# Optimization experiments

Measured on AMD Instinct MI355X. Metric: run time of the kernel, lower is better.

## Reference

```python
import math
import jax, jax.numpy as jnp
import numpy as np

B, S, D, H = 2, 2048, 1024, 16
DK = D // H


def setup_inputs() -> dict:
    key = jax.random.key(0)
    ks = jax.random.split(key, 12)
    scale = 1.0 / math.sqrt(D)
    inp = {
        "q": jax.random.normal(ks[0], (B, S, D), jnp.float32),
        "k": jax.random.normal(ks[1], (B, S, D), jnp.float32),
        "v": jax.random.normal(ks[2], (B, S, D), jnp.float32),
        # causal mask, broadcast over batch and heads (mask==0 -> -inf)
        "mask": jnp.tril(jnp.ones((S, S), jnp.int32))[None, None, :, :],
        "Wq": jax.random.normal(ks[3], (D, D), jnp.float32) * scale,
        "bq": jnp.zeros((D,), jnp.float32),
        "Wk": jax.random.normal(ks[4], (D, D), jnp.float32) * scale,
        "bk": jnp.zeros((D,), jnp.float32),
        "Wv": jax.random.normal(ks[5], (D, D), jnp.float32) * scale,
        "bv": jnp.zeros((D,), jnp.float32),
        "Wo": jax.random.normal(ks[6], (D, D), jnp.float32) * scale,
        "bo": jnp.zeros((D,), jnp.float32),
    }
    return inp


def reference(q, k, v, mask, Wq, bq, Wk, bk, Wv, bv, Wo, bo):
    def proj(x, W, b):
        # [B,S,D] -> [B,H,S,DK]
        return (x @ W + b).reshape(B, -1, H, DK).transpose(0, 2, 1, 3)

    Q = proj(q, Wq, bq)
    K = proj(k, Wk, bk)
    V = proj(v, Wv, bv)
    scores = jnp.einsum("bhqd,bhkd->bhqk", Q, K) / math.sqrt(DK)  # [B,H,S,S]
    scores = jnp.where(mask == 0, -jnp.inf, scores)
    attn = jax.nn.softmax(scores, axis=-1)  # dropout p=0.0 -> identity
    ctx = jnp.einsum("bhqk,bhkd->bhqd", attn, V)
    ctx = ctx.transpose(0, 2, 1, 3).reshape(B, -1, D)  # [B,S,D]
    return ctx @ Wo + bo
```

## Files before the change

### kernel.cpp

```cpp
#include <hip/hip_runtime.h>
#include <stdint.h>

#define BB 2
#define SS 2048
#define DD 1024
#define HH 16
#define DK 64

#define QSCALE 0.1803368801111204f
#define NEGS -1.0e30f

typedef short s16x8 __attribute__((ext_vector_type(8)));
typedef float f32x4 __attribute__((ext_vector_type(4)));
typedef unsigned short u16x4 __attribute__((ext_vector_type(4)));
typedef unsigned int u32x4 __attribute__((ext_vector_type(4)));

static __device__ __forceinline__ unsigned short f2bf(float f) {
  unsigned int u = __builtin_bit_cast(unsigned int, f);
  u = (u + 0x7fffu + ((u >> 16) & 1u)) >> 16;
  return (unsigned short)u;
}

static __device__ __forceinline__ unsigned int cvtpk(float lo, float hi) {
  unsigned int r;
  asm("v_cvt_pk_bf16_f32 %0, %1, %2" : "=v"(r) : "v"(lo), "v"(hi));
  return r;
}

static __device__ __forceinline__ f32x4 mfma16(s16x8 a, s16x8 b, f32x4 c) {
  return __builtin_amdgcn_mfma_f32_16x16x32_bf16(a, b, c, 0, 0, 0);
}

static __device__ __forceinline__ void gload_lds16(const void* g, void* l) {
  __builtin_amdgcn_global_load_lds(
      (const __attribute__((address_space(1))) unsigned int*)g,
      (__attribute__((address_space(3))) unsigned int*)l, 16, 0, 0);
}

__global__ __launch_bounds__(256) void cvt3_kernel(const float* __restrict__ q,
                                                   const float* __restrict__ k,
                                                   const float* __restrict__ v,
                                                   unsigned short* __restrict__ qb,
                                                   unsigned short* __restrict__ kb,
                                                   unsigned short* __restrict__ vb) {
  int sel = blockIdx.y;
  const float* in = (sel == 0) ? q : ((sel == 1) ? k : v);
  unsigned short* out = (sel == 0) ? qb : ((sel == 1) ? kb : vb);
  int i = blockIdx.x * 256 + threadIdx.x;
  f32x4 vv = ((const f32x4*)in)[i];
  u16x4 o;
  o.x = f2bf(vv.x); o.y = f2bf(vv.y); o.z = f2bf(vv.z); o.w = f2bf(vv.w);
  ((u16x4*)out)[i] = o;
}

__global__ __launch_bounds__(256) void transpose_w4_kernel(const float* __restrict__ Wq,
                                                           const float* __restrict__ Wk,
                                                           const float* __restrict__ Wv,
                                                           const float* __restrict__ Wo,
                                                           unsigned short* __restrict__ WTbase) {
  __shared__ float t[32][33];
  int z = blockIdx.z;
  const float* W = (z == 0) ? Wq : ((z == 1) ? Wk : ((z == 2) ? Wv : Wo));
  float scale = (z == 0) ? QSCALE : 1.0f;
  unsigned short* WT = WTbase + (size_t)z * DD * DD;
  int n0 = blockIdx.x * 32, k0 = blockIdx.y * 32;
  int tx = threadIdx.x, ty = threadIdx.y;
  for (int i = 0; i < 4; ++i)
    t[ty + 8 * i][tx] = W[(size_t)(k0 + ty + 8 * i) * DD + n0 + tx];
  __syncthreads();
  for (int i = 0; i < 4; ++i)
    WT[(size_t)(n0 + ty + 8 * i) * DD + k0 + tx] = f2bf(t[tx][ty + 8 * i] * scale);
}

__global__ __launch_bounds__(256) void transpose_v_kernel(const unsigned short* __restrict__ V,
                                                          unsigned short* __restrict__ VT) {
  __shared__ unsigned short t[32][33];
  int s0 = blockIdx.x * 32, d0 = blockIdx.y * 32, bh = blockIdx.z;
  int tx = threadIdx.x, ty = threadIdx.y;
  const unsigned short* Vb = V + (size_t)bh * SS * DK;
  unsigned short* Tb = VT + (size_t)bh * DK * SS;
  for (int i = 0; i < 4; ++i)
    t[ty + 8 * i][tx] = Vb[(size_t)(s0 + ty + 8 * i) * DK + d0 + tx];
  __syncthreads();
  for (int i = 0; i < 4; ++i)
    Tb[(size_t)(d0 + ty + 8 * i) * SS + s0 + tx] = t[tx][ty + 8 * i];
}

__global__ __launch_bounds__(256) void gemm_qkv_kernel(
    const unsigned short* __restrict__ qb, const unsigned short* __restrict__ kb,
    const unsigned short* __restrict__ vb, const unsigned short* __restrict__ WTbase,
    const float* __restrict__ bq, const float* __restrict__ bk,
    const float* __restrict__ bv, unsigned short* __restrict__ Qh,
    unsigned short* __restrict__ Kh, unsigned short* __restrict__ Vh) {
  const int K = DD;
  __shared__ __align__(16) unsigned short Alds[128 * 32];
  __shared__ __align__(16) unsigned short Blds[128 * 32];
  int tid = threadIdx.x;
  int lane = tid & 63, wave = tid >> 6;
  int g = lane >> 4, r16 = lane & 15;
  int seg = blockIdx.y >> 5;
  int m0 = (blockIdx.y & 31) * 128, n0 = blockIdx.x * 128;
  int wm = (wave >> 1) * 64, wn = (wave & 1) * 64;

  const unsigned short* A = (seg == 0) ? qb : ((seg == 1) ? kb : vb);
  const unsigned short* BT = WTbase + (size_t)seg * DD * DD;
  const float* bias = (seg == 0) ? bq : ((seg == 1) ? bk : bv);
  unsigned short* outh = (seg == 0) ? Qh : ((seg == 1) ? Kh : Vh);
  float bsc = (seg == 0) ? QSCALE : 1.0f;

  f32x4 acc[4][4] = {};

  int c0 = tid, c1 = tid + 256;
  int arow0 = c0 >> 2, arow1 = c1 >> 2;
  int as0 = (c0 & 3) ^ ((arow0 >> 1) & 3);
  int as1 = (c1 & 3) ^ ((arow1 >> 1) & 3);

  for (int k0 = 0; k0 < K; k0 += 32) {
    __syncthreads();
    gload_lds16((const char*)(A + (size_t)(m0 + arow0) * K + k0) + as0 * 16,
                (char*)Alds + wave * 1024);
    gload_lds16((const char*)(A + (size_t)(m0 + arow1) * K + k0) + as1 * 16,
                (char*)Alds + wave * 1024 + 4096);
    gload_lds16((const char*)(BT + (size_t)(n0 + arow0) * K + k0) + as0 * 16,
                (char*)Blds + wave * 1024);
    gload_lds16((const char*)(BT + (size_t)(n0 + arow1) * K + k0) + as1 * 16,
                (char*)Blds + wave * 1024 + 4096);
    __syncthreads();

    s16x8 af[4], bfr[4];
#pragma unroll
    for (int mt = 0; mt < 4; ++mt) {
      int row = wm + mt * 16 + r16;
      int ch = g ^ ((row >> 1) & 3);
      af[mt] = *(const s16x8*)((const char*)Alds + row * 64 + ch * 16);
    }
#pragma unroll
    for (int nt = 0; nt < 4; ++nt) {
      int row = wn + nt * 16 + r16;
      int ch = g ^ ((row >> 1) & 3);
      bfr[nt] = *(const s16x8*)((const char*)Blds + row * 64 + ch * 16);
    }
#pragma unroll
    for (int mt = 0; mt < 4; ++mt)
#pragma unroll
      for (int nt = 0; nt < 4; ++nt)
        acc[mt][nt] = mfma16(af[mt], bfr[nt], acc[mt][nt]);
  }

#pragma unroll
  for (int nt = 0; nt < 4; ++nt) {
    int col = n0 + wn + nt * 16 + r16;
    int h = col >> 6, dk = col & (DK - 1);
    float bvv = bias[col] * bsc;
#pragma unroll
    for (int mt = 0; mt < 4; ++mt) {
#pragma unroll
      for (int rr = 0; rr < 4; ++rr) {
        int rowg = m0 + wm + mt * 16 + g * 4 + rr;
        int bb = rowg >> 11, s = rowg & (SS - 1);
        float val = acc[mt][nt][rr] + bvv;
        outh[(((size_t)bb * HH + h) * SS + s) * DK + dk] = f2bf(val);
      }
    }
  }
}

__global__ __launch_bounds__(256) void gemm_out_kernel(const unsigned short* __restrict__ A,
                                                       const unsigned short* __restrict__ BT,
                                                       const float* __restrict__ bias,
                                                       float* __restrict__ out) {
  const int K = DD;
  __shared__ __align__(16) unsigned short Alds[128 * 32];
  __shared__ __align__(16) unsigned short Blds[64 * 32];
  int tid = threadIdx.x;
  int lane = tid & 63, wave = tid >> 6;
  int g = lane >> 4, r16 = lane & 15;
  int m0 = blockIdx.y * 128, n0 = blockIdx.x * 64;
  int wm = (wave >> 1) * 64, wn = (wave & 1) * 32;

  f32x4 acc[4][2] = {};

  int c0 = tid, c1 = tid + 256;
  int arow0 = c0 >> 2, arow1 = c1 >> 2;
  int as0 = (c0 & 3) ^ ((arow0 >> 1) & 3);
  int as1 = (c1 & 3) ^ ((arow1 >> 1) & 3);

  for (int k0 = 0; k0 < K; k0 += 32) {
    __syncthreads();
    gload_lds16((const char*)(A + (size_t)(m0 + arow0) * K + k0) + as0 * 16,
                (char*)Alds + wave * 1024);
    gload_lds16((const char*)(A + (size_t)(m0 + arow1) * K + k0) + as1 * 16,
                (char*)Alds + wave * 1024 + 4096);
    gload_lds16((const char*)(BT + (size_t)(n0 + arow0) * K + k0) + as0 * 16,
                (char*)Blds + wave * 1024);
    __syncthreads();

    s16x8 af[4], bfr[2];
#pragma unroll
    for (int mt = 0; mt < 4; ++mt) {
      int row = wm + mt * 16 + r16;
      int ch = g ^ ((row >> 1) & 3);
      af[mt] = *(const s16x8*)((const char*)Alds + row * 64 + ch * 16);
    }
#pragma unroll
    for (int nt = 0; nt < 2; ++nt) {
      int row = wn + nt * 16 + r16;
      int ch = g ^ ((row >> 1) & 3);
      bfr[nt] = *(const s16x8*)((const char*)Blds + row * 64 + ch * 16);
    }
#pragma unroll
    for (int mt = 0; mt < 4; ++mt)
#pragma unroll
      for (int nt = 0; nt < 2; ++nt)
        acc[mt][nt] = mfma16(af[mt], bfr[nt], acc[mt][nt]);
  }

#pragma unroll
  for (int nt = 0; nt < 2; ++nt) {
    int col = n0 + wn + nt * 16 + r16;
    float bvv = bias[col];
#pragma unroll
    for (int mt = 0; mt < 4; ++mt) {
#pragma unroll
      for (int rr = 0; rr < 4; ++rr) {
        int rowg = m0 + wm + mt * 16 + g * 4 + rr;
        out[(size_t)rowg * DD + col] = acc[mt][nt][rr] + bvv;
      }
    }
  }
}

__global__ __launch_bounds__(256) void attn_kernel(const unsigned short* __restrict__ Qh,
                                                   const unsigned short* __restrict__ Kh,
                                                   const unsigned short* __restrict__ VhT,
                                                   unsigned short* __restrict__ ctx) {
  __shared__ __align__(16) unsigned short Klds[3][64 * 64];
  __shared__ __align__(16) unsigned short Vlds[3][64 * 64];

  int tid = threadIdx.x;
  int lane = tid & 63, wave = tid >> 6;
  int g = lane >> 4, r16 = lane & 15;
  int bid = blockIdx.x;
  int bh = ((bid >> 7) << 3) | (bid & 7);
  int pid = (bid >> 3) & 15;

  const int NTQ = SS / 64;
  int q0A = pid * 64, q0B = (NTQ - 1 - pid) * 64;
  int tilesA = pid + 1;
  int NT = NTQ + 1;

  const unsigned short* Qb = Qh + (size_t)bh * SS * DK;
  const char* Kb = (const char*)(Kh + (size_t)bh * SS * DK);
  const char* Vb = (const char*)(VhT + (size_t)bh * DK * SS);

  int a_ = r16 >> 2, b_ = r16 & 3;
  int rbase = 8 * a_ + b_;
  int sk = b_ + 4 * (a_ & 1);

  int c0 = tid, c1 = tid + 256;
  int row0 = c0 >> 3, row1 = c1 >> 3;
  int skst0 = ((row0 & 3) | (((row0 >> 3) & 1) << 2));
  int skst1 = ((row1 & 3) | (((row1 >> 3) & 1) << 2));
  int kc0 = (c0 & 7) ^ skst0, kc1 = (c1 & 7) ^ skst1;
  int vc0 = (c0 & 7) ^ (row0 & 7), vc1 = (c1 & 7) ^ (row1 & 7);

#define KV_OF(t) ((((t) >= tilesA) ? (t) - tilesA : (t)) * 64)
#define STAGE_KV(buf, kv0)                                                   \
  do {                                                                       \
    gload_lds16(Kb + ((size_t)((kv0) + row0) * 128) + kc0 * 16,              \
                (char*)Klds[buf] + wave * 1024);                             \
    gload_lds16(Kb + ((size_t)((kv0) + row1) * 128) + kc1 * 16,              \
                (char*)Klds[buf] + wave * 1024 + 4096);                      \
    gload_lds16(Vb + ((size_t)row0 * SS + (kv0)) * 2 + vc0 * 16,             \
                (char*)Vlds[buf] + wave * 1024);                             \
    gload_lds16(Vb + ((size_t)row1 * SS + (kv0)) * 2 + vc1 * 16,             \
                (char*)Vlds[buf] + wave * 1024 + 4096);                      \
  } while (0)

  int b = bh >> 4, h = bh & (HH - 1);

  int qw0 = q0A + wave * 16;
  s16x8 aq[2];
#pragma unroll
  for (int kc = 0; kc < 2; ++kc)
    aq[kc] = *(const s16x8*)(Qb + (size_t)(qw0 + r16) * DK + kc * 32 + g * 8);

  STAGE_KV(0, 0);
  STAGE_KV(1, KV_OF(1));

  f32x4 accd[4] = {};
  float mrow = -INFINITY, lrow = 0.0f;
  u16x4 outA[4];
  int srowA = 0;

  for (int t = 0; t < NT; ++t) {
    if (t == tilesA) {
      float inv = 1.0f / lrow;
      srowA = qw0 + r16;
#pragma unroll
      for (int dsub = 0; dsub < 4; ++dsub)
#pragma unroll
        for (int rr = 0; rr < 4; ++rr) outA[dsub][rr] = f2bf(accd[dsub][rr] * inv);
      qw0 = q0B + wave * 16;
#pragma unroll
      for (int kc = 0; kc < 2; ++kc)
        aq[kc] = *(const s16x8*)(Qb + (size_t)(qw0 + r16) * DK + kc * 32 + g * 8);
#pragma unroll
      for (int dsub = 0; dsub < 4; ++dsub) accd[dsub] = (f32x4){0.f, 0.f, 0.f, 0.f};
      mrow = -INFINITY;
      lrow = 0.0f;
    }

    int kv0 = KV_OF(t);

    if (t < NT - 1)
      asm volatile("s_waitcnt vmcnt(4)" ::: "memory");
    else
      asm volatile("s_waitcnt vmcnt(0)" ::: "memory");
    __builtin_amdgcn_s_barrier();
    __builtin_amdgcn_sched_barrier(0);
    if (t + 2 < NT) STAGE_KV((t + 2) % 3, KV_OF(t + 2));

    const char* Kc = (const char*)Klds[t % 3];
    const char* Vc = (const char*)Vlds[t % 3];

    f32x4 sf[4] = {};
    __builtin_amdgcn_s_setprio(1);
#pragma unroll
    for (int kc = 0; kc < 2; ++kc) {
      s16x8 bk[4];
#pragma unroll
      for (int nt = 0; nt < 4; ++nt) {
        int row = rbase + 4 * (nt & 1) + 32 * (nt >> 1);
        int ch = (kc * 4 + g) ^ sk;
        bk[nt] = *(const s16x8*)(Kc + row * 128 + ch * 16);
      }
#pragma unroll
      for (int nt = 0; nt < 4; ++nt)
        sf[nt] = mfma16(bk[nt], aq[kc], sf[nt]);
    }
    __builtin_amdgcn_s_setprio(0);

    s16x8 av[2][4];
#pragma unroll
    for (int c = 0; c < 2; ++c)
#pragma unroll
      for (int dsub = 0; dsub < 4; ++dsub) {
        int row = dsub * 16 + r16;
        int ch = (c * 4 + g) ^ (row & 7);
        av[c][dsub] = *(const s16x8*)(Vc + row * 128 + ch * 16);
      }

    if (kv0 + 63 > qw0) {
      int thr = qw0 + r16 - kv0 - 8 * g;
#pragma unroll
      for (int nt = 0; nt < 4; ++nt) {
        int koff = 4 * (nt & 1) + 32 * (nt >> 1);
#pragma unroll
        for (int rr = 0; rr < 4; ++rr)
          if (koff + rr > thr) sf[nt][rr] = NEGS;
      }
    }

    float tmax = NEGS;
#pragma unroll
    for (int nt = 0; nt < 4; ++nt)
#pragma unroll
      for (int rr = 0; rr < 4; ++rr) tmax = fmaxf(tmax, sf[nt][rr]);
    tmax = fmaxf(tmax, __shfl_xor(tmax, 16));
    tmax = fmaxf(tmax, __shfl_xor(tmax, 32));

    if (!__all(tmax <= mrow)) {
      float mn = fmaxf(mrow, tmax);
      float fc = __builtin_amdgcn_exp2f(mrow - mn);
      lrow *= fc;
      mrow = mn;
#pragma unroll
      for (int dsub = 0; dsub < 4; ++dsub)
#pragma unroll
        for (int rr = 0; rr < 4; ++rr) accd[dsub][rr] *= fc;
    }

    float pf[4][4];
    float su = 0.0f;
#pragma unroll
    for (int nt = 0; nt < 4; ++nt)
#pragma unroll
      for (int rr = 0; rr < 4; ++rr) {
        float p = __builtin_amdgcn_exp2f(sf[nt][rr] - mrow);
        pf[nt][rr] = p;
        su += p;
      }
    su += __shfl_xor(su, 16);
    su += __shfl_xor(su, 32);
    lrow += su;

    unsigned int pk[2][4];
#pragma unroll
    for (int c = 0; c < 2; ++c) {
      pk[c][0] = cvtpk(pf[2 * c][0], pf[2 * c][1]);
      pk[c][1] = cvtpk(pf[2 * c][2], pf[2 * c][3]);
      pk[c][2] = cvtpk(pf[2 * c + 1][0], pf[2 * c + 1][1]);
      pk[c][3] = cvtpk(pf[2 * c + 1][2], pf[2 * c + 1][3]);
    }

    __builtin_amdgcn_s_setprio(1);
#pragma unroll
    for (int c = 0; c < 2; ++c) {
      s16x8 pb = __builtin_bit_cast(s16x8, *(u32x4*)pk[c]);
#pragma unroll
      for (int dsub = 0; dsub < 4; ++dsub)
        accd[dsub] = mfma16(av[c][dsub], pb, accd[dsub]);
    }
    __builtin_amdgcn_s_setprio(0);
  }

#pragma unroll
  for (int dsub = 0; dsub < 4; ++dsub) {
    int d0 = dsub * 16 + 4 * g;
    *(u16x4*)&ctx[(((size_t)b * SS + srowA) * HH + h) * DK + d0] = outA[dsub];
  }
  int srow = qw0 + r16;
  float inv = 1.0f / lrow;
#pragma unroll
  for (int dsub = 0; dsub < 4; ++dsub) {
    int d0 = dsub * 16 + 4 * g;
    u16x4 o;
#pragma unroll
    for (int rr = 0; rr < 4; ++rr) o[rr] = f2bf(accd[dsub][rr] * inv);
    *(u16x4*)&ctx[(((size_t)b * SS + srow) * HH + h) * DK + d0] = o;
  }
#undef STAGE_KV
#undef KV_OF
}

extern "C" void kernel_launch(void* const* d_in, const int* in_sizes, int n_in,
                              void* d_out, int out_size, void* d_ws, size_t ws_size,
                              hipStream_t stream) {
  const float* q = (const float*)d_in[0];
  const float* k = (const float*)d_in[1];
  const float* v = (const float*)d_in[2];
  const float* Wq = (const float*)d_in[4];
  const float* bq = (const float*)d_in[5];
  const float* Wk = (const float*)d_in[6];
  const float* bk = (const float*)d_in[7];
  const float* Wv = (const float*)d_in[8];
  const float* bv = (const float*)d_in[9];
  const float* Wo = (const float*)d_in[10];
  const float* bo = (const float*)d_in[11];

  char* ws = (char*)d_ws;
  const size_t MB = 1ull << 20;
  unsigned short* qb = (unsigned short*)(ws + 0 * MB);
  unsigned short* kb = (unsigned short*)(ws + 8 * MB);
  unsigned short* vb = (unsigned short*)(ws + 16 * MB);
  unsigned short* WTbase = (unsigned short*)(ws + 24 * MB);
  unsigned short* WoT = (unsigned short*)(ws + 30 * MB);
  unsigned short* Qh = (unsigned short*)(ws + 32 * MB);
  unsigned short* Kh = (unsigned short*)(ws + 40 * MB);
  unsigned short* Vh = (unsigned short*)(ws + 48 * MB);
  unsigned short* VhT = (unsigned short*)(ws + 16 * MB);
  unsigned short* ctx = (unsigned short*)(ws + 0 * MB);

  const int n4 = BB * SS * DD / 4;

  cvt3_kernel<<<dim3(n4 / 256, 3), 256, 0, stream>>>(q, k, v, qb, kb, vb);

  dim3 tb(32, 8);
  transpose_w4_kernel<<<dim3(32, 32, 4), tb, 0, stream>>>(Wq, Wk, Wv, Wo, WTbase);

  gemm_qkv_kernel<<<dim3(8, 96), 256, 0, stream>>>(qb, kb, vb, WTbase,
                                                   bq, bk, bv, Qh, Kh, Vh);

  transpose_v_kernel<<<dim3(SS / 32, DK / 32, BB * HH), tb, 0, stream>>>(Vh, VhT);

  attn_kernel<<<512, 256, 0, stream>>>(Qh, Kh, VhT, ctx);

  gemm_out_kernel<<<dim3(16, 32), 256, 0, stream>>>(ctx, WoT, bo, (float*)d_out);
}
```

Baseline: 130.4 us.

## Split attention KV range across two blocks and merge partials in combine kernel

Each attention work item is split in two along the KV axis, doubling the grid to 1024 blocks with roughly half the tiles each. Each half writes a normalized bf16 partial output plus its (max, sum) statistics. A new combine kernel rescales and merges the two partials into ctx. The K/V staging also drops from a three-deep LDS buffer with explicit vmcnt waits to a two-deep buffer behind __syncthreads. The aim is more parallelism and occupancy, at the cost of an extra launch, extra partial-output traffic and a shallower prefetch pipeline.

```diff
diff --git a/kernel.cpp b/kernel.cpp
--- a/kernel.cpp
+++ b/kernel.cpp
@@ -19,6 +19,11 @@
   unsigned int u = __builtin_bit_cast(unsigned int, f);
   u = (u + 0x7fffu + ((u >> 16) & 1u)) >> 16;
   return (unsigned short)u;
+}
+
+static __device__ __forceinline__ float bf2f(unsigned short s) {
+  unsigned int u = ((unsigned int)s) << 16;
+  return __builtin_bit_cast(float, u);
 }
 
 static __device__ __forceinline__ unsigned int cvtpk(float lo, float hi) {
@@ -233,21 +238,25 @@
 __global__ __launch_bounds__(256) void attn_kernel(const unsigned short* __restrict__ Qh,
                                                    const unsigned short* __restrict__ Kh,
                                                    const unsigned short* __restrict__ VhT,
-                                                   unsigned short* __restrict__ ctx) {
-  __shared__ __align__(16) unsigned short Klds[3][64 * 64];
-  __shared__ __align__(16) unsigned short Vlds[3][64 * 64];
+                                                   unsigned short* __restrict__ ctx,
+                                                   unsigned short* __restrict__ Opart,
+                                                   float2* __restrict__ mlpart) {
+  __shared__ __align__(16) unsigned short Klds[2][64 * 64];
+  __shared__ __align__(16) unsigned short Vlds[2][64 * 64];
 
   int tid = threadIdx.x;
   int lane = tid & 63, wave = tid >> 6;
   int g = lane >> 4, r16 = lane & 15;
   int bid = blockIdx.x;
-  int bh = ((bid >> 7) << 3) | (bid & 7);
-  int pid = (bid >> 3) & 15;
-
-  const int NTQ = SS / 64;
-  int q0A = pid * 64, q0B = (NTQ - 1 - pid) * 64;
-  int tilesA = pid + 1;
-  int NT = NTQ + 1;
+  int x = bid >> 3;
+  int pid = x & 15;
+  int hf = (x >> 4) & 1;
+  int bh = ((x >> 5) << 3) | (bid & 7);
+
+  int tilesA = hf ? 0 : pid + 1;
+  int NT = hf ? 16 : 17;
+  int q0A = pid * 64, q0B = (31 - pid) * 64;
+  int kvoffB = hf ? (16 - pid) : 0;
 
   const unsigned short* Qb = Qh + (size_t)bh * SS * DK;
   const char* Kb = (const char*)(Kh + (size_t)bh * SS * DK);
@@ -264,7 +273,7 @@
   int kc0 = (c0 & 7) ^ skst0, kc1 = (c1 & 7) ^ skst1;
   int vc0 = (c0 & 7) ^ (row0 & 7), vc1 = (c1 & 7) ^ (row1 & 7);
 
-#define KV_OF(t) ((((t) >= tilesA) ? (t) - tilesA : (t)) * 64)
+#define KV_OF(t) ((hf ? (kvoffB + (t)) : (((t) < tilesA) ? (t) : ((t) - tilesA))) * 64)
 #define STAGE_KV(buf, kv0)                                                   \
   do {                                                                       \
     gload_lds16(Kb + ((size_t)((kv0) + row0) * 128) + kc0 * 16,              \
@@ -279,28 +288,29 @@
 
   int b = bh >> 4, h = bh & (HH - 1);
 
-  int qw0 = q0A + wave * 16;
+  int qw0 = (hf ? q0B : q0A) + wave * 16;
   s16x8 aq[2];
 #pragma unroll
   for (int kc = 0; kc < 2; ++kc)
     aq[kc] = *(const s16x8*)(Qb + (size_t)(qw0 + r16) * DK + kc * 32 + g * 8);
 
-  STAGE_KV(0, 0);
-  STAGE_KV(1, KV_OF(1));
+  STAGE_KV(0, KV_OF(0));
 
   f32x4 accd[4] = {};
   float mrow = -INFINITY, lrow = 0.0f;
-  u16x4 outA[4];
-  int srowA = 0;
 
   for (int t = 0; t < NT; ++t) {
-    if (t == tilesA) {
+    if (hf == 0 && t == tilesA) {
       float inv = 1.0f / lrow;
-      srowA = qw0 + r16;
-#pragma unroll
-      for (int dsub = 0; dsub < 4; ++dsub)
-#pragma unroll
-        for (int rr = 0; rr < 4; ++rr) outA[dsub][rr] = f2bf(accd[dsub][rr] * inv);
+      int srow = qw0 + r16;
+#pragma unroll
+      for (int dsub = 0; dsub < 4; ++dsub) {
+        int d0 = dsub * 16 + 4 * g;
+        u16x4 o;
+#pragma unroll
+        for (int rr = 0; rr < 4; ++rr) o[rr] = f2bf(accd[dsub][rr] * inv);
+        *(u16x4*)&ctx[(((size_t)b * SS + srow) * HH + h) * DK + d0] = o;
+      }
       qw0 = q0B + wave * 16;
 #pragma unroll
       for (int kc = 0; kc < 2; ++kc)
@@ -313,16 +323,11 @@
 
     int kv0 = KV_OF(t);
 
-    if (t < NT - 1)
-      asm volatile("s_waitcnt vmcnt(4)" ::: "memory");
-    else
-      asm volatile("s_waitcnt vmcnt(0)" ::: "memory");
-    __builtin_amdgcn_s_barrier();
-    __builtin_amdgcn_sched_barrier(0);
-    if (t + 2 < NT) STAGE_KV((t + 2) % 3, KV_OF(t + 2));
-
-    const char* Kc = (const char*)Klds[t % 3];
-    const char* Vc = (const char*)Vlds[t % 3];
+    __syncthreads();
+    if (t + 1 < NT) STAGE_KV((t + 1) & 1, KV_OF(t + 1));
+
+    const char* Kc = (const char*)Klds[t & 1];
+    const char* Vc = (const char*)Vlds[t & 1];
 
     f32x4 sf[4] = {};
     __builtin_amdgcn_s_setprio(1);
@@ -415,23 +420,46 @@
     __builtin_amdgcn_s_setprio(0);
   }
 
-#pragma unroll
-  for (int dsub = 0; dsub < 4; ++dsub) {
-    int d0 = dsub * 16 + 4 * g;
-    *(u16x4*)&ctx[(((size_t)b * SS + srowA) * HH + h) * DK + d0] = outA[dsub];
-  }
-  int srow = qw0 + r16;
+  size_t prow = ((size_t)bh * 16 + pid) * 64 + wave * 16 + r16;
   float inv = 1.0f / lrow;
+  unsigned short* Op = Opart + ((size_t)hf * 32768 + prow) * 64;
 #pragma unroll
   for (int dsub = 0; dsub < 4; ++dsub) {
     int d0 = dsub * 16 + 4 * g;
     u16x4 o;
 #pragma unroll
     for (int rr = 0; rr < 4; ++rr) o[rr] = f2bf(accd[dsub][rr] * inv);
-    *(u16x4*)&ctx[(((size_t)b * SS + srow) * HH + h) * DK + d0] = o;
+    *(u16x4*)&Op[d0] = o;
   }
+  if (g == 0) mlpart[(size_t)hf * 32768 + prow] = make_float2(mrow, lrow);
 #undef STAGE_KV
 #undef KV_OF
+}
+
+__global__ __launch_bounds__(256) void combine_kernel(const unsigned short* __restrict__ Opart,
+                                                      const float2* __restrict__ mlpart,
+                                                      unsigned short* __restrict__ ctx) {
+  int idx = blockIdx.x * 256 + threadIdx.x;
+  int row = idx >> 4;
+  int d0 = (idx & 15) * 4;
+  float2 ml0 = mlpart[row];
+  float2 ml1 = mlpart[32768 + row];
+  float m = fmaxf(ml0.x, ml1.x);
+  float w0 = __builtin_amdgcn_exp2f(ml0.x - m) * ml0.y;
+  float w1 = __builtin_amdgcn_exp2f(ml1.x - m) * ml1.y;
+  float inv = 1.0f / (w0 + w1);
+  w0 *= inv;
+  w1 *= inv;
+  u16x4 a = *(const u16x4*)(Opart + (size_t)row * 64 + d0);
+  u16x4 bb4 = *(const u16x4*)(Opart + ((size_t)32768 + row) * 64 + d0);
+  u16x4 o;
+#pragma unroll
+  for (int j = 0; j < 4; ++j) o[j] = f2bf(bf2f(a[j]) * w0 + bf2f(bb4[j]) * w1);
+  int p = row >> 6, rin = row & 63;
+  int bh = p >> 4, pid = p & 15;
+  int srow = (31 - pid) * 64 + rin;
+  int b = bh >> 4, h = bh & (HH - 1);
+  *(u16x4*)&ctx[(((size_t)b * SS + srow) * HH + h) * DK + d0] = o;
 }
 
 extern "C" void kernel_launch(void* const* d_in, const int* in_sizes, int n_in,
@@ -461,6 +489,8 @@
   unsigned short* Vh = (unsigned short*)(ws + 48 * MB);
   unsigned short* VhT = (unsigned short*)(ws + 16 * MB);
   unsigned short* ctx = (unsigned short*)(ws + 0 * MB);
+  unsigned short* Opart = (unsigned short*)(ws + 8 * MB);
+  float2* mlpart = (float2*)(ws + 24 * MB);
 
   const int n4 = BB * SS * DD / 4;
 
@@ -474,7 +504,9 @@
 
   transpose_v_kernel<<<dim3(SS / 32, DK / 32, BB * HH), tb, 0, stream>>>(Vh, VhT);
 
-  attn_kernel<<<512, 256, 0, stream>>>(Qh, Kh, VhT, ctx);
+  attn_kernel<<<1024, 256, 0, stream>>>(Qh, Kh, VhT, ctx, Opart, mlpart);
+
+  combine_kernel<<<2048, 256, 0, stream>>>(Opart, mlpart, ctx);
 
   gemm_out_kernel<<<dim3(16, 32), 256, 0, stream>>>(ctx, WoT, bo, (float*)d_out);
 }
```

After: 132.9 us. Within noise of the previous version (+2.0%).
